# Performance work log

Measured on AMD Instinct MI355X. Metric: run time of the kernel, lower is better.

Reference implementation:

```python
import jax, jax.numpy as jnp
import numpy as np

N = 10000      # nodes
E = 160000     # edges
B = 4          # batch
D = 256        # in_dim == out_dim
H = 4          # heads
DH = D // H    # per-head dim = 64
L = 2          # num_layers
BACK = 2       # back_look
HID = 128      # hidden_dim
NEG = 0.1      # leaky relu slope


def setup_inputs() -> dict:
    key = jax.random.key(0)
    ks = jax.random.split(key, 12)
    solutions = jax.random.normal(ks[0], (BACK, B, N, HID), dtype=jnp.float32)
    src = jax.random.randint(ks[1], (E,), 0, N)
    dst = jax.random.randint(ks[2], (E,), 0, N)
    w = jax.random.uniform(ks[3], (E,), dtype=jnp.float32)
    fc_w = jax.random.normal(ks[4], (L, D, D), dtype=jnp.float32) * (1.0 / np.sqrt(D))
    attn_l = jax.random.normal(ks[5], (L, H, DH), dtype=jnp.float32) * 0.1
    attn_r = jax.random.normal(ks[6], (L, H, DH), dtype=jnp.float32) * 0.1
    out_fc_w = jax.random.normal(ks[7], (L, DH, DH), dtype=jnp.float32) * (1.0 / np.sqrt(DH))
    out_fc_b = jnp.zeros((L, DH), dtype=jnp.float32)
    mlp_w = jax.random.normal(ks[8], (D, L * D), dtype=jnp.float32) * (1.0 / np.sqrt(L * D))
    mlp_b = jnp.zeros((D,), dtype=jnp.float32)
    return dict(solutions=solutions, w=w, fc_w=fc_w, attn_l=attn_l, attn_r=attn_r,
                out_fc_w=out_fc_w, out_fc_b=out_fc_b, mlp_w=mlp_w, mlp_b=mlp_b,
                src=src, dst=dst)


def _gat_layer(x, w, fc_w, al, ar, ofc_w, ofc_b, src, dst):
    # x: [B,N,D] -> feat: [N,B,H,DH]  (matches torch view+transpose)
    feat = jnp.einsum('bnd,ed->bne', x, fc_w).reshape(B, N, H, DH).transpose(1, 0, 2, 3)
    el = (feat * al).sum(-1)  # [N,B,H]
    er = (feat * ar).sum(-1)  # [N,B,H]
    # edge scores, weighted pre-softmax by edge weight w
    e = jax.nn.leaky_relu(el[src] + er[dst], NEG) * w[:, None, None]  # [E,B,H]
    # edge softmax per destination node (numerically stable)
    m = jax.ops.segment_max(e, dst, num_segments=N)        # [N,B,H]
    ex = jnp.exp(e - m[dst])
    s = jax.ops.segment_sum(ex, dst, num_segments=N)       # [N,B,H]
    a = ex / s[dst]                                        # [E,B,H]
    # weighted scatter-aggregate: u_mul_e + sum
    msg = feat[src] * a[..., None]                         # [E,B,H,DH]
    rst = jax.ops.segment_sum(msg, dst, num_segments=N)    # [N,B,H,DH]
    rst = jax.nn.relu(jnp.einsum('nbhf,of->nbho', rst, ofc_w) + ofc_b)
    # transpose + concat heads -> [B,N,H*DH]
    return rst.transpose(1, 0, 2, 3).reshape(B, N, H * DH)


def reference(solutions, w, fc_w, attn_l, attn_r, out_fc_w, out_fc_b, mlp_w, mlp_b, src, dst):
    # concat back_look solutions along feature dim -> [B,N,D]
    x = jnp.concatenate([solutions[i] for i in range(BACK)], axis=-1)
    outs = []
    for l in range(L):
        x = _gat_layer(x, w, fc_w[l], attn_l[l], attn_r[l],
                       out_fc_w[l], out_fc_b[l], src, dst)
        outs.append(x)
    h = jnp.concatenate(outs, axis=-1)           # [B,N,L*D]
    return h @ mlp_w.T + mlp_b                   # [B,N,D]
```

## Files before the change

kernel.cpp:

```cpp
#include <hip/hip_runtime.h>
#include <math.h>

#define NN 10000
#define NE 160000
#define NB 4
#define NH 4
#define ND 256
#define NT (NN * 16)
#define NM 40000

typedef _Float16 f16;
typedef _Float16 half8 __attribute__((ext_vector_type(8)));
typedef _Float16 h2 __attribute__((ext_vector_type(2)));
typedef float f32x4 __attribute__((ext_vector_type(4)));

union H4 { uint2 u; f16 h[4]; };
union U2H { unsigned u; h2 h; };
union U4H { uint4 u; h2 h[4]; };

__device__ __forceinline__ void gload_lds16(const void* g, void* l) {
  __builtin_amdgcn_global_load_lds((const __attribute__((address_space(1))) void*)g,
                                   (__attribute__((address_space(3))) void*)l, 16, 0, 0);
}

__global__ __launch_bounds__(256) void k_deg(const int* __restrict__ dst, int* __restrict__ deg) {
  int e = blockIdx.x * 256 + threadIdx.x;
  if (e < NE) atomicAdd(&deg[dst[e]], 1);
}

__global__ __launch_bounds__(1024) void k_scan2(const int* __restrict__ deg, int* __restrict__ offs) {
  __shared__ int wsum[16];
  __shared__ int wbase[17];
  const int t = threadIdx.x, lane = t & 63, wv = t >> 6;
  int v[10];
  int s = 0;
  if (t < 1000) {
#pragma unroll
    for (int i = 0; i < 10; ++i) { v[i] = deg[t * 10 + i]; s += v[i]; }
  }
  int inc = s;
#pragma unroll
  for (int k = 1; k < 64; k <<= 1) {
    int u = __shfl_up(inc, k);
    if (lane >= k) inc += u;
  }
  if (lane == 63) wsum[wv] = inc;
  __syncthreads();
  if (t == 0) {
    int c = 0;
#pragma unroll
    for (int i = 0; i < 16; ++i) { wbase[i] = c; c += wsum[i]; }
    wbase[16] = c;
    offs[NN] = c;
  }
  __syncthreads();
  if (t < 1000) {
    int c = wbase[wv] + inc - s;
#pragma unroll
    for (int i = 0; i < 10; ++i) { offs[t * 10 + i] = c; c += v[i]; }
  }
}

__global__ __launch_bounds__(256) void k_scatter(const int* __restrict__ src, const int* __restrict__ dst,
                                                 const float* __restrict__ w, const int* __restrict__ offs,
                                                 int* __restrict__ cursor, int* __restrict__ csr_src,
                                                 float* __restrict__ csr_w) {
  int e = blockIdx.x * 256 + threadIdx.x;
  if (e < NE) {
    int d = dst[e];
    int slot = offs[d] + atomicAdd(&cursor[d], 1);
    csr_src[slot] = src[e];
    csr_w[slot] = w[e];
  }
}

__global__ __launch_bounds__(256) void k_prep(const float* __restrict__ fc_w, const float* __restrict__ ofc_w,
                                              const float* __restrict__ al, const float* __restrict__ ar,
                                              const float* __restrict__ mlp_w,
                                              f16* __restrict__ fwh2, f16* __restrict__ alfh2,
                                              f16* __restrict__ mlph) {
  int r = blockIdx.x;
  int d = threadIdx.x;
  if (r < 512) {
    int l = r >> 8, rr = r & 255;
    int h = rr >> 6, o = rr & 63;
    const float* fcl = fc_w + (size_t)l * 65536;
    const float* ow = ofc_w + (size_t)l * 4096;
    float acc = 0.f;
    for (int f = 0; f < 64; ++f)
      acc = fmaf(ow[(o << 6) + f], fcl[(((h << 6) + f) << 8) + d], acc);
    fwh2[((size_t)l << 16) + (rr << 8) + d] = (f16)acc;
  } else if (r < 544) {
    int rr = r - 512;
    int l = rr >> 4, q = rr & 15;
    const float* fcl = fc_w + (size_t)l * 65536;
    float acc = 0.f;
    if (q < 8) {
      int h = q & 3;
      const float* a = ((q < 4) ? al : ar) + (size_t)l * NH * 64;
      for (int f = 0; f < 64; ++f)
        acc = fmaf(a[(h << 6) + f], fcl[(((h << 6) + f) << 8) + d], acc);
    }
    alfh2[((size_t)l << 12) + (q << 8) + d] = (f16)acc;
  } else {
    int i = (r - 544) * 256 + d;
    float4 v = *(const float4*)(mlp_w + (size_t)i * 4);
    H4 h;
    h.h[0] = (f16)v.x; h.h[1] = (f16)v.y; h.h[2] = (f16)v.z; h.h[3] = (f16)v.w;
    *(uint2*)(mlph + (size_t)i * 4) = h.u;
  }
}

template<int OUTH, int EL, int CVT>
__global__ __launch_bounds__(256) void k_gemm_f16(
    const void* __restrict__ A, int lda, int K,
    const f16* __restrict__ W,
    const float* __restrict__ bias,
    void* __restrict__ outp, int ldo,
    const f16* __restrict__ alfh, float* __restrict__ el2, float* __restrict__ er2)
{
  __shared__ __align__(16) f16 As[64 * 32];
  __shared__ __align__(16) f16 Bs[128 * 32];
  const int tid = threadIdx.x;
  const int lane = tid & 63;
  const int w = tid >> 6;
  const int wr = w >> 1, wc = w & 1;
  const int ra0 = blockIdx.x * 64;
  const int c0 = blockIdx.y * 128;
  const int l2 = lane >> 2;
  const int lk8 = (lane & 3) * 8;

  f32x4 acc[2][4];
#pragma unroll
  for (int mr = 0; mr < 2; ++mr)
#pragma unroll
    for (int nr = 0; nr < 4; ++nr) acc[mr][nr] = (f32x4)0.f;
  f32x4 accel[2];
  accel[0] = (f32x4)0.f; accel[1] = (f32x4)0.f;
  const bool doEl = EL && (blockIdx.y == 0) && (wc == 0);

  const int fr = lane & 15;
  const int fg = (lane >> 4) * 8;

  for (int k0 = 0; k0 < K; k0 += 32) {
    if (CVT) {
      const float* sf = (const float*)A;
      int ra = ra0 + 16 * w + l2;
      int kk = k0 + lk8;
      const float* ps = (kk < 128) ? sf + (size_t)ra * 128 + kk
                                   : sf + (size_t)(NM + ra) * 128 + (kk - 128);
      float4 p0 = *(const float4*)ps;
      float4 p1 = *(const float4*)(ps + 4);
      half8 hv;
      hv[0] = (f16)p0.x; hv[1] = (f16)p0.y; hv[2] = (f16)p0.z; hv[3] = (f16)p0.w;
      hv[4] = (f16)p1.x; hv[5] = (f16)p1.y; hv[6] = (f16)p1.z; hv[7] = (f16)p1.w;
      *(half8*)(As + w * 512 + (lane << 3)) = hv;
    } else {
      gload_lds16((const f16*)A + (size_t)(ra0 + 16 * w + l2) * lda + k0 + lk8, As + w * 512);
    }
    gload_lds16(W + (size_t)(c0 + 32 * w + l2) * K + k0 + lk8, Bs + w * 1024);
    gload_lds16(W + (size_t)(c0 + 32 * w + 16 + l2) * K + k0 + lk8, Bs + w * 1024 + 512);
    __syncthreads();

    half8 af[2], bf[4];
#pragma unroll
    for (int mr = 0; mr < 2; ++mr)
      af[mr] = *(const half8*)(As + (wr * 32 + mr * 16 + fr) * 32 + fg);
#pragma unroll
    for (int nr = 0; nr < 4; ++nr)
      bf[nr] = *(const half8*)(Bs + (wc * 64 + nr * 16 + fr) * 32 + fg);
#pragma unroll
    for (int mr = 0; mr < 2; ++mr)
#pragma unroll
      for (int nr = 0; nr < 4; ++nr)
        acc[mr][nr] = __builtin_amdgcn_mfma_f32_16x16x32_f16(af[mr], bf[nr], acc[mr][nr], 0, 0, 0);
    if (doEl) {
      half8 bal = *(const half8*)(alfh + fr * 256 + k0 + fg);
#pragma unroll
      for (int mr = 0; mr < 2; ++mr)
        accel[mr] = __builtin_amdgcn_mfma_f32_16x16x32_f16(af[mr], bal, accel[mr], 0, 0, 0);
    }
    __syncthreads();
  }

  const int r0 = (lane >> 4) * 4;
#pragma unroll
  for (int nr = 0; nr < 4; ++nr) {
    int col = c0 + wc * 64 + nr * 16 + fr;
    float bv = bias ? bias[col] : 0.f;
#pragma unroll
    for (int mr = 0; mr < 2; ++mr) {
      f32x4 v = acc[mr][nr];
#pragma unroll
      for (int r = 0; r < 4; ++r) {
        int ra = ra0 + wr * 32 + mr * 16 + r0 + r;
        float val = v[r] + bv;
        if (OUTH) ((f16*)outp)[(size_t)ra * ldo + col] = (f16)val;
        else      ((float*)outp)[(size_t)ra * ldo + col] = val;
      }
    }
  }
  if (doEl && fr < 8) {
#pragma unroll
    for (int mr = 0; mr < 2; ++mr) {
#pragma unroll
      for (int r = 0; r < 4; ++r) {
        int ra = ra0 + wr * 32 + mr * 16 + r0 + r;
        int n = ra % NN, b = ra / NN;
        int tb = (n << 4) + (b << 2);
        float val = accel[mr][r];
        if (fr < 4) el2[tb + fr] = val;
        else        er2[tb + (fr - 4)] = val;
      }
    }
  }
}

__global__ __launch_bounds__(256) void k_soft(
    const int* __restrict__ csr_src, const float* __restrict__ csr_w,
    const int* __restrict__ offs,
    const float* __restrict__ el2, const float* __restrict__ er2,
    unsigned* __restrict__ exsp, float* __restrict__ sinv)
{
  const int t = threadIdx.x;
  const int w = t >> 6, lane = t & 63;
  const int n = blockIdx.x * 4 + w;
  const int bh = lane & 15, es = lane >> 4;
  const int b = bh >> 2, h = bh & 3;
  const int s0 = offs[n], s1 = offs[n + 1];
  const float erv = er2[(n << 4) + bh];

  float m = -INFINITY;
  for (int e = s0 + es; e < s1; e += 4) {
    int src = csr_src[e];
    float x = el2[(src << 4) + bh] + erv;
    x = (x > 0.f) ? x : 0.1f * x;
    m = fmaxf(m, x * csr_w[e]);
  }
  m = fmaxf(m, __shfl_xor(m, 16));
  m = fmaxf(m, __shfl_xor(m, 32));

  float ps = 0.f;
  for (int e = s0 + es; e < s1; e += 4) {
    int src = csr_src[e];
    float x = el2[(src << 4) + bh] + erv;
    x = (x > 0.f) ? x : 0.1f * x;
    float a = __expf(x * csr_w[e] - m);
    f16 ah = (f16)a;
    U2H sp; sp.h[0] = ah; sp.h[1] = ah;
    exsp[(((size_t)b * NE + e) << 2) + h] = sp.u;
    ps += a;
  }
  ps += __shfl_xor(ps, 16);
  ps += __shfl_xor(ps, 32);
  if (es == 0) sinv[(((size_t)b * NN + n) << 2) + h] = (s1 > s0) ? 1.f / ps : 0.f;
}

__global__ __launch_bounds__(256) void k_edge7(
    const f16* __restrict__ featW_b, const unsigned* __restrict__ exsp,
    const float* __restrict__ sinv, const int* __restrict__ csr_src,
    const int* __restrict__ offs, const float* __restrict__ b2, f16* __restrict__ outh)
{
  __shared__ __align__(16) unsigned aalp[4][64][4];
  __shared__ unsigned asrc[4][64];
  const int t = threadIdx.x;
  const int w = t >> 6, lane = t & 63;
  const int b = blockIdx.x & 3;
  const int n = (blockIdx.x >> 2) * 4 + w;
  const int s0 = offs[n], s1 = offs[n + 1];
  const int hl = lane & 31;
  const int eh = lane >> 5;
  const int h8 = hl >> 3;
  const int ch0 = hl << 3;
  const f16* fW = featW_b + ((size_t)b * NN << 8);
  const unsigned* exb = exsp + ((size_t)b * NE << 2);

  h2 a0 = {(f16)0.f, (f16)0.f}, a1 = a0, a2 = a0, a3 = a0;

  for (int c0 = s0; c0 < s1; c0 += 64) {
    const int csz = min(64, s1 - c0);
    unsigned sv = 0;
    uint4 av = {0u, 0u, 0u, 0u};
    if (lane < csz) {
      sv = (unsigned)csr_src[c0 + lane];
      av = *(const uint4*)(exb + ((size_t)(c0 + lane) << 2));
    }
    asrc[w][lane] = sv;
    *(uint4*)(&aalp[w][lane][0]) = av;
#pragma unroll 2
    for (int e = 0; e < csz; e += 2) {
      const int ee = e + eh;
      unsigned su = asrc[w][ee];
      U2H al; al.u = aalp[w][ee][h8];
      U4H fv;
      fv.u = *(const uint4*)(fW + ((size_t)su << 8) + ch0);
      a0 += fv.h[0] * al.h;
      a1 += fv.h[1] * al.h;
      a2 += fv.h[2] * al.h;
      a3 += fv.h[3] * al.h;
    }
  }
  U2H u0, u1, u2, u3;
  u0.h = a0; u1.h = a1; u2.h = a2; u3.h = a3;
  U2H p0, p1, p2, p3;
  p0.u = (unsigned)__shfl_xor((int)u0.u, 32);
  p1.u = (unsigned)__shfl_xor((int)u1.u, 32);
  p2.u = (unsigned)__shfl_xor((int)u2.u, 32);
  p3.u = (unsigned)__shfl_xor((int)u3.u, 32);
  a0 += p0.h; a1 += p1.h; a2 += p2.h; a3 += p3.h;

  if (lane < 32) {
    const float invv = sinv[(((size_t)b * NN + n) << 2) + h8];
    const float4 bv0 = *(const float4*)(b2 + ((hl & 7) << 3));
    const float4 bv1 = *(const float4*)(b2 + ((hl & 7) << 3) + 4);
    H4 o01, o23;
    o01.h[0] = (f16)fmaxf(fmaf((float)a0[0], invv, bv0.x), 0.f);
    o01.h[1] = (f16)fmaxf(fmaf((float)a0[1], invv, bv0.y), 0.f);
    o01.h[2] = (f16)fmaxf(fmaf((float)a1[0], invv, bv0.z), 0.f);
    o01.h[3] = (f16)fmaxf(fmaf((float)a1[1], invv, bv0.w), 0.f);
    o23.h[0] = (f16)fmaxf(fmaf((float)a2[0], invv, bv1.x), 0.f);
    o23.h[1] = (f16)fmaxf(fmaf((float)a2[1], invv, bv1.y), 0.f);
    o23.h[2] = (f16)fmaxf(fmaf((float)a3[0], invv, bv1.z), 0.f);
    o23.h[3] = (f16)fmaxf(fmaf((float)a3[1], invv, bv1.w), 0.f);
    uint4 ov;
    ov.x = o01.u.x; ov.y = o01.u.y; ov.z = o23.u.x; ov.w = o23.u.y;
    *(uint4*)(outh + ((size_t)(b * NN + n) << 9) + ch0) = ov;
  }
}

extern "C" void kernel_launch(void* const* d_in, const int* in_sizes, int n_in,
                              void* d_out, int out_size, void* d_ws, size_t ws_size,
                              hipStream_t stream) {
  const float* sol    = (const float*)d_in[0];
  const float* w      = (const float*)d_in[1];
  const float* fc_w   = (const float*)d_in[2];
  const float* attn_l = (const float*)d_in[3];
  const float* attn_r = (const float*)d_in[4];
  const float* ofc_w  = (const float*)d_in[5];
  const float* ofc_b  = (const float*)d_in[6];
  const float* mlp_w  = (const float*)d_in[7];
  const float* mlp_b  = (const float*)d_in[8];
  const int*   d_src  = (const int*)d_in[9];
  const int*   d_dst  = (const int*)d_in[10];
  float* out = (float*)d_out;

  char* p = (char*)d_ws;
  auto alloc = [&](size_t bytes) { char* r = p; p += (bytes + 255) & ~(size_t)255; return r; };
  f16*   out01h  = (f16*)alloc((size_t)(NM + 128) * 512 * 2);
  f16*   featWb  = (f16*)alloc((size_t)NM * 256 * 2);
  f16*   fwh2    = (f16*)alloc((size_t)2 * ND * ND * 2);
  f16*   alfh2   = (f16*)alloc((size_t)2 * 16 * ND * 2);
  f16*   mlph    = (f16*)alloc((size_t)ND * 512 * 2);
  float* el2     = (float*)alloc((size_t)NT * 4);
  float* er2     = (float*)alloc((size_t)NT * 4);
  unsigned* exsp = (unsigned*)alloc((size_t)4 * NE * 4 * 4 + 4096);
  float* sinv    = (float*)alloc((size_t)NT * 4);
  int*   deg     = (int*)alloc((size_t)(NN + 1) * 4);
  int*   offs    = (int*)alloc((size_t)(NN + 1) * 4);
  int*   cursor  = (int*)alloc((size_t)NN * 4);
  int*   csr_src = (int*)alloc((size_t)NE * 4);
  float* csr_w   = (float*)alloc((size_t)NE * 4);
  if ((size_t)(p - (char*)d_ws) > ws_size) return;

  hipMemsetAsync(deg, 0, (size_t)NN * 4, stream);
  hipMemsetAsync(cursor, 0, (size_t)NN * 4, stream);
  k_deg<<<NE / 256, 256, 0, stream>>>(d_dst, deg);
  k_scan2<<<1, 1024, 0, stream>>>(deg, offs);
  k_scatter<<<NE / 256, 256, 0, stream>>>(d_src, d_dst, w, offs, cursor, csr_src, csr_w);

  k_prep<<<672, 256, 0, stream>>>(fc_w, ofc_w, attn_l, attn_r, mlp_w, fwh2, alfh2, mlph);

  for (int l = 0; l < 2; ++l) {
    const f16* fwh  = fwh2 + ((size_t)l << 16);
    const f16* alfh = alfh2 + ((size_t)l << 12);
    if (l == 0) {
      k_gemm_f16<1, 1, 1><<<dim3(NM / 64, ND / 128), 256, 0, stream>>>(
          sol, 128, 256, fwh, nullptr, featWb, 256, alfh, el2, er2);
    } else {
      k_gemm_f16<1, 1, 0><<<dim3(NM / 64, ND / 128), 256, 0, stream>>>(
          out01h, 512, 256, fwh, nullptr, featWb, 256, alfh, el2, er2);
    }
    k_soft<<<NN / 4, 256, 0, stream>>>(csr_src, csr_w, offs, el2, er2, exsp, sinv);
    k_edge7<<<(NN / 4) * 4, 256, 0, stream>>>(featWb, exsp, sinv, csr_src, offs,
                                              ofc_b + (size_t)l * 64, out01h + (l == 0 ? 0 : 256));
  }

  k_gemm_f16<0, 0, 0><<<dim3(NM / 64, ND / 128), 256, 0, stream>>>(
      out01h, 512, 512, mlph, mlp_b, out, 256, nullptr, nullptr, nullptr);
}
```

Measured before the change: 189.7 us.

## Fuse edge softmax into aggregation kernel with online max and rescaling

Removes the separate softmax kernel and its exsp/sinv intermediate buffers. The aggregation kernel now computes edge scores per 64-edge chunk, keeps a running max and sum (online softmax), and rescales the fp16 accumulators whenever the max changes. This cuts one launch per layer and the global write and read of the per-edge exp values. In exchange the scores are computed per block, and the fp16 accumulator rescaling adds some error. LDS is read right after being written within the wave, with no barrier between.

```diff
diff --git a/kernel.cpp b/kernel.cpp
--- a/kernel.cpp
+++ b/kernel.cpp
@@ -216,77 +216,78 @@
   }
 }
 
-__global__ __launch_bounds__(256) void k_soft(
+__global__ __launch_bounds__(256) void k_edge8(
+    const f16* __restrict__ featW_b, const float* __restrict__ el2, const float* __restrict__ er2,
     const int* __restrict__ csr_src, const float* __restrict__ csr_w,
-    const int* __restrict__ offs,
-    const float* __restrict__ el2, const float* __restrict__ er2,
-    unsigned* __restrict__ exsp, float* __restrict__ sinv)
-{
-  const int t = threadIdx.x;
-  const int w = t >> 6, lane = t & 63;
-  const int n = blockIdx.x * 4 + w;
-  const int bh = lane & 15, es = lane >> 4;
-  const int b = bh >> 2, h = bh & 3;
-  const int s0 = offs[n], s1 = offs[n + 1];
-  const float erv = er2[(n << 4) + bh];
-
-  float m = -INFINITY;
-  for (int e = s0 + es; e < s1; e += 4) {
-    int src = csr_src[e];
-    float x = el2[(src << 4) + bh] + erv;
-    x = (x > 0.f) ? x : 0.1f * x;
-    m = fmaxf(m, x * csr_w[e]);
-  }
-  m = fmaxf(m, __shfl_xor(m, 16));
-  m = fmaxf(m, __shfl_xor(m, 32));
-
-  float ps = 0.f;
-  for (int e = s0 + es; e < s1; e += 4) {
-    int src = csr_src[e];
-    float x = el2[(src << 4) + bh] + erv;
-    x = (x > 0.f) ? x : 0.1f * x;
-    float a = __expf(x * csr_w[e] - m);
-    f16 ah = (f16)a;
-    U2H sp; sp.h[0] = ah; sp.h[1] = ah;
-    exsp[(((size_t)b * NE + e) << 2) + h] = sp.u;
-    ps += a;
-  }
-  ps += __shfl_xor(ps, 16);
-  ps += __shfl_xor(ps, 32);
-  if (es == 0) sinv[(((size_t)b * NN + n) << 2) + h] = (s1 > s0) ? 1.f / ps : 0.f;
-}
-
-__global__ __launch_bounds__(256) void k_edge7(
-    const f16* __restrict__ featW_b, const unsigned* __restrict__ exsp,
-    const float* __restrict__ sinv, const int* __restrict__ csr_src,
     const int* __restrict__ offs, const float* __restrict__ b2, f16* __restrict__ outh)
 {
   __shared__ __align__(16) unsigned aalp[4][64][4];
   __shared__ unsigned asrc[4][64];
+  __shared__ float aw[4][64];
+  __shared__ float sls[4][4];
+  __shared__ float sinvs[4][4];
   const int t = threadIdx.x;
   const int w = t >> 6, lane = t & 63;
   const int b = blockIdx.x & 3;
   const int n = (blockIdx.x >> 2) * 4 + w;
   const int s0 = offs[n], s1 = offs[n + 1];
+  const int es = lane >> 2;
+  const int sh = lane & 3;
+  const float erv = er2[(n << 4) + (b << 2) + sh];
   const int hl = lane & 31;
   const int eh = lane >> 5;
   const int h8 = hl >> 3;
   const int ch0 = hl << 3;
   const f16* fW = featW_b + ((size_t)b * NN << 8);
-  const unsigned* exb = exsp + ((size_t)b * NE << 2);
-
+
+  float m = -INFINITY, srun = 0.f;
   h2 a0 = {(f16)0.f, (f16)0.f}, a1 = a0, a2 = a0, a3 = a0;
 
   for (int c0 = s0; c0 < s1; c0 += 64) {
     const int csz = min(64, s1 - c0);
     unsigned sv = 0;
-    uint4 av = {0u, 0u, 0u, 0u};
+    float wv = 0.f;
     if (lane < csz) {
       sv = (unsigned)csr_src[c0 + lane];
-      av = *(const uint4*)(exb + ((size_t)(c0 + lane) << 2));
+      wv = csr_w[c0 + lane];
     }
     asrc[w][lane] = sv;
-    *(uint4*)(&aalp[w][lane][0]) = av;
+    aw[w][lane] = wv;
+    float sc[4];
+#pragma unroll
+    for (int i = 0; i < 4; ++i) {
+      int e = es + 16 * i;
+      if (e < csz) {
+        int src = (int)asrc[w][e];
+        float x = el2[(src << 4) + (b << 2) + sh] + erv;
+        x = (x > 0.f) ? x : 0.1f * x;
+        sc[i] = x * aw[w][e];
+      } else sc[i] = -INFINITY;
+    }
+    float mc = fmaxf(fmaxf(sc[0], sc[1]), fmaxf(sc[2], sc[3]));
+#pragma unroll
+    for (int k = 4; k <= 32; k <<= 1) mc = fmaxf(mc, __shfl_xor(mc, k));
+    float mn = fmaxf(m, mc);
+    float sl = (m == -INFINITY) ? 0.f : __expf(m - mn);
+    float ps = 0.f;
+#pragma unroll
+    for (int i = 0; i < 4; ++i) {
+      int e = es + 16 * i;
+      float a = (e < csz) ? __expf(sc[i] - mn) : 0.f;
+      ps += a;
+      f16 ah = (f16)a;
+      U2H sp; sp.h[0] = ah; sp.h[1] = ah;
+      aalp[w][e][sh] = sp.u;
+    }
+#pragma unroll
+    for (int k = 4; k <= 32; k <<= 1) ps += __shfl_xor(ps, k);
+    srun = srun * sl + ps;
+    m = mn;
+    if (es == 0) sls[w][sh] = sl;
+    float slA = sls[w][h8];
+    f16 slh = (f16)slA;
+    h2 slv = {slh, slh};
+    a0 *= slv; a1 *= slv; a2 *= slv; a3 *= slv;
 #pragma unroll 2
     for (int e = 0; e < csz; e += 2) {
       const int ee = e + eh;
@@ -309,8 +310,11 @@
   p3.u = (unsigned)__shfl_xor((int)u3.u, 32);
   a0 += p0.h; a1 += p1.h; a2 += p2.h; a3 += p3.h;
 
+  float invs = (s1 > s0) ? 1.f / srun : 0.f;
+  if (es == 0) sinvs[w][sh] = invs;
+
   if (lane < 32) {
-    const float invv = sinv[(((size_t)b * NN + n) << 2) + h8];
+    const float invv = sinvs[w][h8];
     const float4 bv0 = *(const float4*)(b2 + ((hl & 7) << 3));
     const float4 bv1 = *(const float4*)(b2 + ((hl & 7) << 3) + 4);
     H4 o01, o23;
@@ -353,8 +357,6 @@
   f16*   mlph    = (f16*)alloc((size_t)ND * 512 * 2);
   float* el2     = (float*)alloc((size_t)NT * 4);
   float* er2     = (float*)alloc((size_t)NT * 4);
-  unsigned* exsp = (unsigned*)alloc((size_t)4 * NE * 4 * 4 + 4096);
-  float* sinv    = (float*)alloc((size_t)NT * 4);
   int*   deg     = (int*)alloc((size_t)(NN + 1) * 4);
   int*   offs    = (int*)alloc((size_t)(NN + 1) * 4);
   int*   cursor  = (int*)alloc((size_t)NN * 4);
@@ -380,8 +382,7 @@
       k_gemm_f16<1, 1, 0><<<dim3(NM / 64, ND / 128), 256, 0, stream>>>(
           out01h, 512, 256, fwh, nullptr, featWb, 256, alfh, el2, er2);
     }
-    k_soft<<<NN / 4, 256, 0, stream>>>(csr_src, csr_w, offs, el2, er2, exsp, sinv);
-    k_edge7<<<(NN / 4) * 4, 256, 0, stream>>>(featWb, exsp, sinv, csr_src, offs,
+    k_edge8<<<(NN / 4) * 4, 256, 0, stream>>>(featWb, el2, er2, csr_src, csr_w, offs,
                                               ofc_b + (size_t)l * 64, out01h + (l == 0 ? 0 : 256));
   }
 
```

Result: faster. 185.3 us (-2.3%).
